# Kernel optimization log

Measured on AMD Instinct MI355X. Metric: run time of the kernel, lower is better.

Reference implementation:

```python
import jax, jax.numpy as jnp
import numpy as np

EMBED = 1024
HEADS = 16
HEAD_DIM = EMBED // HEADS


def setup_inputs() -> dict:
    key = jax.random.key(0)
    ks = jax.random.split(key, 5)
    s = 1.0 / np.sqrt(EMBED)
    return {
        "x": jax.random.normal(ks[0], (4, 2048, EMBED), dtype=jnp.float32),
        "W_qkv": jax.random.uniform(ks[1], (EMBED, 3 * EMBED), jnp.float32, -s, s),
        "b_qkv": jax.random.uniform(ks[2], (3 * EMBED,), jnp.float32, -s, s),
        "W_out": jax.random.uniform(ks[3], (EMBED, EMBED), jnp.float32, -s, s),
        "b_out": jax.random.uniform(ks[4], (EMBED,), jnp.float32, -s, s),
    }


def reference(x, W_qkv, b_qkv, W_out, b_out):
    B, S, E = x.shape
    qkv = x @ W_qkv + b_qkv  # [B,S,3E]
    q, k, v = jnp.split(qkv, 3, axis=-1)
    # [B,S,E] -> [B,H,S,D]
    def split_heads(t):
        return t.reshape(B, S, HEADS, HEAD_DIM).transpose(0, 2, 1, 3)
    q, k, v = split_heads(q), split_heads(k), split_heads(v)
    scale = 1.0 / jnp.sqrt(jnp.asarray(HEAD_DIM, dtype=x.dtype))
    scores = jnp.einsum("bhqd,bhkd->bhqk", q, k) * scale
    attn = jax.nn.softmax(scores, axis=-1)
    out = jnp.einsum("bhqk,bhkd->bhqd", attn, v)
    out = out.transpose(0, 2, 1, 3).reshape(B, S, E)
    return out @ W_out + b_out
```

## Files before the change

### kernel.cpp

```cpp
#include <hip/hip_runtime.h>
#include <hip/hip_bf16.h>

typedef __bf16 bf16;
typedef __bf16 bf16x8 __attribute__((ext_vector_type(8)));
typedef float f32x4 __attribute__((ext_vector_type(4)));
typedef float f32x16 __attribute__((ext_vector_type(16)));

#define EMB 1024
#define SEQ 2048
#define NH 16
#define HD 64
#define MTOK 8192

__device__ __forceinline__ void gload16(const bf16* g, bf16* l) {
    __builtin_amdgcn_global_load_lds((const __attribute__((address_space(1))) unsigned int*)g,
                                     (__attribute__((address_space(3))) unsigned int*)l, 16, 0, 0);
}

__global__ __launch_bounds__(256) void prep(const float* __restrict__ x, bf16* __restrict__ xb,
                                            const float* __restrict__ Wq, bf16* __restrict__ WqT,
                                            const float* __restrict__ Wo, bf16* __restrict__ WoT) {
    __shared__ float tile[32][33];
    int bid = blockIdx.x;
    if (bid < 4096) {
        int i = bid * 256 + threadIdx.x;
        const float4* p = (const float4*)x + 2 * (size_t)i;
        float4 a = p[0], b = p[1];
        bf16x8 v;
        v[0] = (bf16)a.x; v[1] = (bf16)a.y; v[2] = (bf16)a.z; v[3] = (bf16)a.w;
        v[4] = (bf16)b.x; v[5] = (bf16)b.y; v[6] = (bf16)b.z; v[7] = (bf16)b.w;
        *(bf16x8*)(xb + 8 * (size_t)i) = v;
        return;
    }
    const float* W;
    bf16* Wt;
    int K = EMB, N, n0, k0;
    if (bid < 4096 + 3072) {
        int i = bid - 4096;
        W = Wq; Wt = WqT; N = 3 * EMB;
        n0 = (i % 96) * 32; k0 = (i / 96) * 32;
    } else {
        int i = bid - 7168;
        W = Wo; Wt = WoT; N = EMB;
        n0 = (i & 31) * 32; k0 = (i >> 5) * 32;
    }
    int tx = threadIdx.x & 31, ty = threadIdx.x >> 5;
    #pragma unroll
    for (int i = 0; i < 32; i += 8)
        tile[ty + i][tx] = W[(size_t)(k0 + ty + i) * N + n0 + tx];
    __syncthreads();
    #pragma unroll
    for (int i = 0; i < 32; i += 8)
        Wt[(size_t)(n0 + ty + i) * K + k0 + tx] = (bf16)tile[tx][ty + i];
}

#define BM 128
#define BN 128
#define BK 64

#define QSCALE 0.1803368801111f

__global__ __launch_bounds__(256) void gemm_qkv(const bf16* __restrict__ A,
                                                const bf16* __restrict__ Bt,
                                                const float* __restrict__ bias,
                                                bf16* __restrict__ qws, bf16* __restrict__ kws,
                                                bf16* __restrict__ vt) {
    __shared__ bf16 sA[BM][BK];
    __shared__ bf16 sB[BN][BK];
    const int K = 1024;
    int lin = blockIdx.x + 64 * blockIdx.y;
    int a8 = lin & 7, tt = lin >> 3;
    int mx = (a8 << 3) + (tt & 7), ny = tt >> 3;
    int m0 = mx * BM, n0 = ny * BN;
    int t = threadIdx.x, lane = t & 63, w = t >> 6;
    int wr = w >> 1, wc = w & 1;
    int l15 = lane & 15, quad = lane >> 4;
    int sw = (l15 & 7) << 3;

    f32x4 acc[4][4];
    #pragma unroll
    for (int i = 0; i < 4; i++)
        #pragma unroll
        for (int j = 0; j < 4; j++) acc[i][j] = (f32x4){0.f, 0.f, 0.f, 0.f};

    int crow = lane >> 3;
    int scol = ((lane & 7) ^ crow) * 8;
    const bf16* gA = A + (size_t)(m0 + w * 32 + crow) * K + scol;
    const bf16* gB = Bt + (size_t)(n0 + w * 32 + crow) * K + scol;

    for (int kt = 0; kt < K; kt += BK) {
        #pragma unroll
        for (int j = 0; j < 4; j++) {
            gload16(gA + (size_t)(j * 8) * K + kt, &sA[w * 32 + j * 8][0]);
            gload16(gB + (size_t)(j * 8) * K + kt, &sB[w * 32 + j * 8][0]);
        }
        __syncthreads();
        #pragma unroll
        for (int ks = 0; ks < BK; ks += 32) {
            int kk = ks + quad * 8;
            int kc = kk ^ sw;
            bf16x8 af[4], bfr[4];
            #pragma unroll
            for (int mt = 0; mt < 4; mt++) af[mt] = *(const bf16x8*)&sA[wr * 64 + mt * 16 + l15][kc];
            #pragma unroll
            for (int nt = 0; nt < 4; nt++) bfr[nt] = *(const bf16x8*)&sB[wc * 64 + nt * 16 + l15][kc];
            #pragma unroll
            for (int mt = 0; mt < 4; mt++)
                #pragma unroll
                for (int nt = 0; nt < 4; nt++)
                    acc[mt][nt] = __builtin_amdgcn_mfma_f32_16x16x32_bf16(af[mt], bfr[nt], acc[mt][nt], 0, 0, 0);
        }
        __syncthreads();
    }
    #pragma unroll
    for (int mt = 0; mt < 4; mt++)
        #pragma unroll
        for (int nt = 0; nt < 4; nt++) {
            int col = n0 + wc * 64 + nt * 16 + l15;
            float bv = bias[col];
            int mat = col >> 10;
            int e = col & 1023;
            int h = e >> 6, d = e & 63;
            int row0 = m0 + wr * 64 + mt * 16 + quad * 4;
            int bb = row0 >> 11, s0 = row0 & 2047;
            int bh = bb * NH + h;
            float vv[4];
            #pragma unroll
            for (int r = 0; r < 4; r++) vv[r] = acc[mt][nt][r] + bv;
            if (mat == 0) {
                #pragma unroll
                for (int r = 0; r < 4; r++)
                    qws[((size_t)bh * SEQ + s0 + r) * HD + d] = (bf16)(vv[r] * QSCALE);
            } else if (mat == 1) {
                #pragma unroll
                for (int r = 0; r < 4; r++)
                    kws[((size_t)bh * SEQ + s0 + r) * HD + d] = (bf16)vv[r];
            } else {
                ushort4 pk;
                pk.x = __builtin_bit_cast(unsigned short, (bf16)vv[0]);
                pk.y = __builtin_bit_cast(unsigned short, (bf16)vv[1]);
                pk.z = __builtin_bit_cast(unsigned short, (bf16)vv[2]);
                pk.w = __builtin_bit_cast(unsigned short, (bf16)vv[3]);
                *(ushort4*)((unsigned short*)vt + ((size_t)bh * HD + d) * SEQ + s0) = pk;
            }
        }
}

__device__ __forceinline__ unsigned pk2(float a, float b) {
    unsigned lo = (unsigned)__builtin_bit_cast(unsigned short, (bf16)a);
    unsigned hi = (unsigned)__builtin_bit_cast(unsigned short, (bf16)b);
    return lo | (hi << 16);
}

__global__ __launch_bounds__(256, 4) void attn(const bf16* __restrict__ qws, const bf16* __restrict__ kws,
                                               const bf16* __restrict__ vt, bf16* __restrict__ ao) {
    __shared__ bf16 sK[2][64][72];
    __shared__ bf16 sVt[2][64][72];

    int lin = blockIdx.x + (SEQ / 128) * blockIdx.y;
    int a8 = lin & 7, tt = lin >> 3;
    int bh = (a8 << 3) + (tt >> 4);
    int q0 = (tt & 15) * 128;
    int t = threadIdx.x, lane = t & 63, w = t >> 6;
    int l31 = lane & 31, hi = lane >> 5;

    const bf16* qb = qws + (size_t)bh * SEQ * HD;
    const bf16* kb = kws + (size_t)bh * SEQ * HD;
    const bf16* vtb = vt + (size_t)bh * HD * SEQ;

    bf16x8 qf[4];
    #pragma unroll
    for (int ks = 0; ks < 4; ks++)
        qf[ks] = *(const bf16x8*)(qb + (size_t)(q0 + w * 32 + l31) * HD + ks * 16 + hi * 8);

    f32x16 o[2];
    float lsum = 0.f;
    #pragma unroll
    for (int mt = 0; mt < 2; mt++)
        #pragma unroll
        for (int r = 0; r < 16; r++) o[mt][r] = 0.f;

    int krow = t >> 3, kc8 = (t & 7) * 8;
    int vdr = t >> 2, vc16 = (t & 3) * 16;

    {
        uint4 k0 = *(const uint4*)(kb + (size_t)krow * HD + kc8);
        uint4 k1 = *(const uint4*)(kb + (size_t)(krow + 32) * HD + kc8);
        const bf16* src = vtb + (size_t)vdr * SEQ + vc16;
        uint4 v0 = *(const uint4*)src;
        uint4 v1 = *(const uint4*)(src + 8);
        *(uint4*)&sK[0][krow][kc8] = k0;
        *(uint4*)&sK[0][krow + 32][kc8] = k1;
        *(uint4*)&sVt[0][vdr][vc16] = v0;
        *(uint4*)&sVt[0][vdr][vc16 + 8] = v1;
    }

    int cur = 0;
    for (int kv0 = 0; kv0 < SEQ; kv0 += 64) {
        __syncthreads();

        int nxt = kv0 + 64;
        uint4 nk0, nk1, nv0, nv1;
        if (nxt < SEQ) {
            nk0 = *(const uint4*)(kb + (size_t)(nxt + krow) * HD + kc8);
            nk1 = *(const uint4*)(kb + (size_t)(nxt + krow + 32) * HD + kc8);
            const bf16* src = vtb + (size_t)vdr * SEQ + nxt + vc16;
            nv0 = *(const uint4*)src;
            nv1 = *(const uint4*)(src + 8);
        }

        f32x16 sacc[2];
        #pragma unroll
        for (int nt = 0; nt < 2; nt++)
            #pragma unroll
            for (int r = 0; r < 16; r++) sacc[nt][r] = 0.f;
        __builtin_amdgcn_s_setprio(1);
        #pragma unroll
        for (int ks = 0; ks < 4; ks++)
            #pragma unroll
            for (int nt = 0; nt < 2; nt++) {
                bf16x8 kf = *(const bf16x8*)&sK[cur][nt * 32 + l31][ks * 16 + hi * 8];
                sacc[nt] = __builtin_amdgcn_mfma_f32_32x32x16_bf16(kf, qf[ks], sacc[nt], 0, 0, 0);
            }
        __builtin_amdgcn_s_setprio(0);

        bf16x8 pb[4];
        #pragma unroll
        for (int nt = 0; nt < 2; nt++) {
            float e[16];
            #pragma unroll
            for (int r = 0; r < 16; r++) {
                e[r] = __builtin_amdgcn_exp2f(sacc[nt][r]);
                lsum += e[r];
            }
            #pragma unroll
            for (int blk = 0; blk < 2; blk++) {
                int b = blk * 8;
                unsigned a0 = pk2(e[b + 0], e[b + 1]);
                unsigned a1 = pk2(e[b + 2], e[b + 3]);
                unsigned b0 = pk2(e[b + 4], e[b + 5]);
                unsigned b1 = pk2(e[b + 6], e[b + 7]);
                asm("v_permlane32_swap_b32 %0, %1" : "+v"(a0), "+v"(b0));
                asm("v_permlane32_swap_b32 %0, %1" : "+v"(a1), "+v"(b1));
                uint4 f;
                f.x = a0; f.y = a1; f.z = b0; f.w = b1;
                pb[nt * 2 + blk] = __builtin_bit_cast(bf16x8, f);
            }
        }

        __builtin_amdgcn_s_setprio(1);
        #pragma unroll
        for (int s = 0; s < 4; s++)
            #pragma unroll
            for (int mt = 0; mt < 2; mt++) {
                bf16x8 vf = *(const bf16x8*)&sVt[cur][mt * 32 + l31][s * 16 + hi * 8];
                o[mt] = __builtin_amdgcn_mfma_f32_32x32x16_bf16(vf, pb[s], o[mt], 0, 0, 0);
            }
        __builtin_amdgcn_s_setprio(0);

        if (nxt < SEQ) {
            *(uint4*)&sK[cur ^ 1][krow][kc8] = nk0;
            *(uint4*)&sK[cur ^ 1][krow + 32][kc8] = nk1;
            *(uint4*)&sVt[cur ^ 1][vdr][vc16] = nv0;
            *(uint4*)&sVt[cur ^ 1][vdr][vc16 + 8] = nv1;
        }
        cur ^= 1;
    }

    float inv = __builtin_amdgcn_rcpf(lsum + __shfl_xor(lsum, 32));

    int h = bh & 15, bb = bh >> 4;
    int q = q0 + w * 32 + l31;
    #pragma unroll
    for (int mt = 0; mt < 2; mt++)
        #pragma unroll
        for (int g = 0; g < 4; g++) {
            ushort4 pk;
            pk.x = __builtin_bit_cast(unsigned short, (bf16)(o[mt][4 * g + 0] * inv));
            pk.y = __builtin_bit_cast(unsigned short, (bf16)(o[mt][4 * g + 1] * inv));
            pk.z = __builtin_bit_cast(unsigned short, (bf16)(o[mt][4 * g + 2] * inv));
            pk.w = __builtin_bit_cast(unsigned short, (bf16)(o[mt][4 * g + 3] * inv));
            *(ushort4*)((unsigned short*)ao + ((size_t)(bb * SEQ + q)) * EMB + h * HD + mt * 32 + 8 * g + 4 * hi) = pk;
        }
}

__global__ __launch_bounds__(256) void gemm_out(const bf16* __restrict__ A,
                                                const bf16* __restrict__ Bt,
                                                const float* __restrict__ bias,
                                                float* __restrict__ out) {
    __shared__ bf16 sA[BM][BK];
    __shared__ bf16 sB[BN][BK];
    const int K = 1024;
    int lin = blockIdx.x + 64 * blockIdx.y;
    int a8 = lin & 7, tt = lin >> 3;
    int mx = (a8 << 3) + (tt & 7), ny = tt >> 3;
    int m0 = mx * BM, n0 = ny * BN;
    int t = threadIdx.x, lane = t & 63, w = t >> 6;
    int wr = w >> 1, wc = w & 1;
    int l15 = lane & 15, quad = lane >> 4;
    int sw = (l15 & 7) << 3;

    f32x4 acc[4][4];
    #pragma unroll
    for (int i = 0; i < 4; i++)
        #pragma unroll
        for (int j = 0; j < 4; j++) acc[i][j] = (f32x4){0.f, 0.f, 0.f, 0.f};

    int crow = lane >> 3;
    int scol = ((lane & 7) ^ crow) * 8;
    const bf16* gA = A + (size_t)(m0 + w * 32 + crow) * K + scol;
    const bf16* gB = Bt + (size_t)(n0 + w * 32 + crow) * K + scol;

    for (int kt = 0; kt < K; kt += BK) {
        #pragma unroll
        for (int j = 0; j < 4; j++) {
            gload16(gA + (size_t)(j * 8) * K + kt, &sA[w * 32 + j * 8][0]);
            gload16(gB + (size_t)(j * 8) * K + kt, &sB[w * 32 + j * 8][0]);
        }
        __syncthreads();
        #pragma unroll
        for (int ks = 0; ks < BK; ks += 32) {
            int kk = ks + quad * 8;
            int kc = kk ^ sw;
            bf16x8 af[4], bfr[4];
            #pragma unroll
            for (int mt = 0; mt < 4; mt++) af[mt] = *(const bf16x8*)&sA[wr * 64 + mt * 16 + l15][kc];
            #pragma unroll
            for (int nt = 0; nt < 4; nt++) bfr[nt] = *(const bf16x8*)&sB[wc * 64 + nt * 16 + l15][kc];
            #pragma unroll
            for (int mt = 0; mt < 4; mt++)
                #pragma unroll
                for (int nt = 0; nt < 4; nt++)
                    acc[mt][nt] = __builtin_amdgcn_mfma_f32_16x16x32_bf16(af[mt], bfr[nt], acc[mt][nt], 0, 0, 0);
        }
        __syncthreads();
    }
    #pragma unroll
    for (int mt = 0; mt < 4; mt++)
        #pragma unroll
        for (int nt = 0; nt < 4; nt++) {
            int col = n0 + wc * 64 + nt * 16 + l15;
            float bv = bias[col];
            #pragma unroll
            for (int r = 0; r < 4; r++) {
                int row = m0 + wr * 64 + mt * 16 + quad * 4 + r;
                out[(size_t)row * EMB + col] = acc[mt][nt][r] + bv;
            }
        }
}

extern "C" void kernel_launch(void* const* d_in, const int* in_sizes, int n_in,
                              void* d_out, int out_size, void* d_ws, size_t ws_size,
                              hipStream_t stream) {
    const float* x     = (const float*)d_in[0];
    const float* W_qkv = (const float*)d_in[1];
    const float* b_qkv = (const float*)d_in[2];
    const float* W_out = (const float*)d_in[3];
    const float* b_out = (const float*)d_in[4];
    float* out = (float*)d_out;

    char* ws = (char*)d_ws;
    bf16* xb    = (bf16*)(ws);
    bf16* wqkvT = (bf16*)(ws + (size_t)(16 << 20));
    bf16* woutT = (bf16*)(ws + (size_t)(22 << 20));
    bf16* qws   = (bf16*)(ws + (size_t)(24 << 20));
    bf16* kws   = (bf16*)(ws + (size_t)(40 << 20));
    bf16* vt    = (bf16*)(ws + (size_t)(56 << 20));
    bf16* aow   = (bf16*)(ws + (size_t)(72 << 20));

    prep<<<8192, 256, 0, stream>>>(x, xb, W_qkv, wqkvT, W_out, woutT);
    gemm_qkv<<<dim3(MTOK / BM, 3 * EMB / BN), 256, 0, stream>>>(xb, wqkvT, b_qkv, qws, kws, vt);
    attn<<<dim3(SEQ / 128, 64), 256, 0, stream>>>(qws, kws, vt, aow);
    gemm_out<<<dim3(MTOK / BM, EMB / BN), 256, 0, stream>>>(aow, woutT, b_out, out);
}
```

Baseline: 259.2 us.

## Stream attention K/V tiles into LDS via direct global_load_lds with XOR swizzle

Replaces the register-staged K/V prefetch (global load into VGPRs, then LDS store after compute) with direct global-to-LDS async loads. Padding is dropped in favour of an XOR swizzle on the 16-byte column chunk to avoid bank conflicts. Sync moves to the end of each iteration. This frees registers and removes the LDS write instructions. The risk is that the single barrier per iteration may not properly wait on the async loads (vmcnt) before the next tile's reads.

```diff
diff --git a/kernel.cpp b/kernel.cpp
--- a/kernel.cpp
+++ b/kernel.cpp
@@ -154,8 +154,8 @@
 
 __global__ __launch_bounds__(256, 4) void attn(const bf16* __restrict__ qws, const bf16* __restrict__ kws,
                                                const bf16* __restrict__ vt, bf16* __restrict__ ao) {
-    __shared__ bf16 sK[2][64][72];
-    __shared__ bf16 sVt[2][64][72];
+    __shared__ bf16 sK[2][64][64];
+    __shared__ bf16 sVt[2][64][64];
 
     int lin = blockIdx.x + (SEQ / 128) * blockIdx.y;
     int a8 = lin & 7, tt = lin >> 3;
@@ -163,6 +163,7 @@
     int q0 = (tt & 15) * 128;
     int t = threadIdx.x, lane = t & 63, w = t >> 6;
     int l31 = lane & 31, hi = lane >> 5;
+    int rsw = (l31 & 7) << 3;
 
     const bf16* qb = qws + (size_t)bh * SEQ * HD;
     const bf16* kb = kws + (size_t)bh * SEQ * HD;
@@ -180,33 +181,26 @@
         #pragma unroll
         for (int r = 0; r < 16; r++) o[mt][r] = 0.f;
 
-    int krow = t >> 3, kc8 = (t & 7) * 8;
-    int vdr = t >> 2, vc16 = (t & 3) * 16;
-
-    {
-        uint4 k0 = *(const uint4*)(kb + (size_t)krow * HD + kc8);
-        uint4 k1 = *(const uint4*)(kb + (size_t)(krow + 32) * HD + kc8);
-        const bf16* src = vtb + (size_t)vdr * SEQ + vc16;
-        uint4 v0 = *(const uint4*)src;
-        uint4 v1 = *(const uint4*)(src + 8);
-        *(uint4*)&sK[0][krow][kc8] = k0;
-        *(uint4*)&sK[0][krow + 32][kc8] = k1;
-        *(uint4*)&sVt[0][vdr][vc16] = v0;
-        *(uint4*)&sVt[0][vdr][vc16 + 8] = v1;
-    }
+    int row8 = lane >> 3;
+    const bf16* gKb = kb + (size_t)(w * 8 + row8) * HD + (((lane & 7) ^ row8) << 3);
+    const bf16* gVb = vtb + (size_t)(w * 8 + row8) * SEQ + (((lane & 7) ^ row8) << 3);
+
+    #pragma unroll
+    for (int p = 0; p < 2; p++) {
+        gload16(gKb + (size_t)(p * 32) * HD, &sK[0][p * 32 + w * 8][0]);
+        gload16(gVb + (size_t)(p * 32) * SEQ, &sVt[0][p * 32 + w * 8][0]);
+    }
+    __syncthreads();
 
     int cur = 0;
     for (int kv0 = 0; kv0 < SEQ; kv0 += 64) {
-        __syncthreads();
-
         int nxt = kv0 + 64;
-        uint4 nk0, nk1, nv0, nv1;
         if (nxt < SEQ) {
-            nk0 = *(const uint4*)(kb + (size_t)(nxt + krow) * HD + kc8);
-            nk1 = *(const uint4*)(kb + (size_t)(nxt + krow + 32) * HD + kc8);
-            const bf16* src = vtb + (size_t)vdr * SEQ + nxt + vc16;
-            nv0 = *(const uint4*)src;
-            nv1 = *(const uint4*)(src + 8);
+            #pragma unroll
+            for (int p = 0; p < 2; p++) {
+                gload16(gKb + (size_t)(nxt + p * 32) * HD, &sK[cur ^ 1][p * 32 + w * 8][0]);
+                gload16(gVb + (size_t)(p * 32) * SEQ + nxt, &sVt[cur ^ 1][p * 32 + w * 8][0]);
+            }
         }
 
         f32x16 sacc[2];
@@ -219,7 +213,7 @@
         for (int ks = 0; ks < 4; ks++)
             #pragma unroll
             for (int nt = 0; nt < 2; nt++) {
-                bf16x8 kf = *(const bf16x8*)&sK[cur][nt * 32 + l31][ks * 16 + hi * 8];
+                bf16x8 kf = *(const bf16x8*)&sK[cur][nt * 32 + l31][(ks * 16 + hi * 8) ^ rsw];
                 sacc[nt] = __builtin_amdgcn_mfma_f32_32x32x16_bf16(kf, qf[ks], sacc[nt], 0, 0, 0);
             }
         __builtin_amdgcn_s_setprio(0);
@@ -253,17 +247,12 @@
         for (int s = 0; s < 4; s++)
             #pragma unroll
             for (int mt = 0; mt < 2; mt++) {
-                bf16x8 vf = *(const bf16x8*)&sVt[cur][mt * 32 + l31][s * 16 + hi * 8];
+                bf16x8 vf = *(const bf16x8*)&sVt[cur][mt * 32 + l31][(s * 16 + hi * 8) ^ rsw];
                 o[mt] = __builtin_amdgcn_mfma_f32_32x32x16_bf16(vf, pb[s], o[mt], 0, 0, 0);
             }
         __builtin_amdgcn_s_setprio(0);
 
-        if (nxt < SEQ) {
-            *(uint4*)&sK[cur ^ 1][krow][kc8] = nk0;
-            *(uint4*)&sK[cur ^ 1][krow + 32][kc8] = nk1;
-            *(uint4*)&sVt[cur ^ 1][vdr][vc16] = nv0;
-            *(uint4*)&sVt[cur ^ 1][vdr][vc16 + 8] = nv1;
-        }
+        __syncthreads();
         cur ^= 1;
     }
 
```

Result: no change. 261.7 us (+0.9%).
